# Kernel optimization log

Measured on AMD Instinct MI355X. Metric: run time of the kernel, lower is better.

Reference implementation:

```python
import jax, jax.numpy as jnp
import numpy as np

N_NODES = 100000
N_EDGES = 3200000
IN_F = 128
OUT_F = 64
HEADS = 8
ALPHA = 0.2  # LeakyReLU negative slope


def setup_inputs() -> dict:
    key = jax.random.key(0)
    k1, k2, k3, k4 = jax.random.split(key, 4)
    x = jax.random.normal(k1, (N_NODES, IN_F), dtype=jnp.float32)
    edges = jax.random.randint(k2, (2, N_EDGES), 0, N_NODES, dtype=jnp.int64)
    # glorot-uniform-ish scaled params, stacked over heads
    lim_W = np.sqrt(6.0 / (IN_F + OUT_F))
    lim_a = np.sqrt(6.0 / (2 * OUT_F + 1))
    W = jax.random.uniform(k3, (HEADS, IN_F, OUT_F), minval=-lim_W, maxval=lim_W, dtype=jnp.float32)
    a = jax.random.uniform(k4, (HEADS, 2 * OUT_F, 1), minval=-lim_a, maxval=lim_a, dtype=jnp.float32)
    return {"x": x, "edges": edges, "W": W, "a": a}


def reference(x, edges, W, a):
    # x: [N, in_f]; edges: [2, E]; W: [H, in_f, out_f]; a: [H, 2*out_f, 1]
    N = x.shape[0]
    src, tgt = edges[0], edges[1]
    outs = []
    for h in range(W.shape[0]):  # small fixed head count; keeps peak memory per-head
        Wh = x @ W[h]                                  # [N, F]
        # Whij @ a == Wh[src] @ a[:F] + Wh[tgt] @ a[F:], computed at node level
        a_src = Wh @ a[h, :OUT_F, 0]                   # [N]
        a_tgt = Wh @ a[h, OUT_F:, 0]                   # [N]
        e = -jax.nn.leaky_relu(a_src[src] + a_tgt[tgt], negative_slope=ALPHA)  # [E]
        e_exp = jnp.exp(e - jnp.max(e))                # global max, as in the torch code
        denom = jax.ops.segment_sum(e_exp, src, num_segments=N) + 1e-10  # [N]
        att = e_exp / denom[src]                       # [E] edge softmax over source groups
        msg = att[:, None] * Wh[tgt]                   # [E, F]
        outs.append(jax.ops.segment_sum(msg, src, num_segments=N))  # [N, F]
    return jnp.concatenate(outs, axis=1)               # concat reduction -> [N, H*F]
```

## Files before the change

kernel.cpp:

```cpp
#include <hip/hip_runtime.h>
#include <hip/hip_bf16.h>

#define N_NODES 100000
#define N_EDGES 3200000
#define IN_F 128
#define OUT_F 64
#define HEADS 8
#define ALPHA 0.2f

#define BSHIFT 7
#define NBUCK 782
#define CHUNK 16384
#define NPBLK 196

typedef __bf16 bf16x8 __attribute__((ext_vector_type(8)));
typedef float f32x4 __attribute__((ext_vector_type(4)));
typedef __attribute__((ext_vector_type(8))) unsigned short ushort8;

static __device__ __forceinline__ unsigned short f2b(float f) {
    __hip_bfloat16 h = __float2bfloat16(f);
    return __builtin_bit_cast(unsigned short, h);
}

static __device__ __forceinline__ void gll16(const void* g, void* l) {
    __builtin_amdgcn_global_load_lds(
        (const __attribute__((address_space(1))) void*)g,
        (__attribute__((address_space(3))) void*)l, 16, 0, 0);
}

__global__ __launch_bounds__(256) void k_prep(const float* __restrict__ W,
                                              const float* __restrict__ a,
                                              unsigned short* __restrict__ Wt,
                                              float* __restrict__ u,
                                              float* __restrict__ v,
                                              int* __restrict__ bhist) {
    int b = blockIdx.x, t = threadIdx.x;
    if (b < 256) {
        int idx = b * 256 + t;
        int k = idx & 127;
        int c = idx >> 7;
        int h = c >> 6;
        int f = c & 63;
        Wt[idx] = f2b(W[h * IN_F * OUT_F + k * OUT_F + f]);
    } else if (b == 256) {
#pragma unroll
        for (int j = 0; j < 4; ++j) {
            int t2 = t + j * 256;
            int h = t2 >> 7, k = t2 & 127;
            const float* Wrow = W + h * IN_F * OUT_F + k * OUT_F;
            const float* ah = a + h * 2 * OUT_F;
            float su = 0.f, sv = 0.f;
            for (int f = 0; f < OUT_F; ++f) {
                float wv = Wrow[f];
                su += wv * ah[f];
                sv += wv * ah[OUT_F + f];
            }
            u[t2] = su;
            v[t2] = sv;
        }
    } else {
        for (int i = t; i < NBUCK; i += 256) bhist[i] = 0;
    }
}

__global__ __launch_bounds__(256) void k_xadot(const float* __restrict__ x,
                                               const float* __restrict__ u,
                                               const float* __restrict__ v,
                                               unsigned short* __restrict__ xb,
                                               float* __restrict__ asrc,
                                               float* __restrict__ atgt) {
    int node = (blockIdx.x * 256 + threadIdx.x) >> 6;
    int lane = threadIdx.x & 63;
    if (node >= N_NODES) return;
    float2 xv = *reinterpret_cast<const float2*>(x + (size_t)node * 128 + 2 * lane);
    ushort2 pv = make_ushort2(f2b(xv.x), f2b(xv.y));
    *reinterpret_cast<ushort2*>(xb + (size_t)node * 128 + 2 * lane) = pv;
    for (int h = 0; h < 8; ++h) {
        float2 uu = *reinterpret_cast<const float2*>(u + h * 128 + 2 * lane);
        float2 vv = *reinterpret_cast<const float2*>(v + h * 128 + 2 * lane);
        float s1 = xv.x * uu.x + xv.y * uu.y;
        float s2 = xv.x * vv.x + xv.y * vv.y;
        for (int d = 1; d < 64; d <<= 1) {
            s1 += __shfl_xor(s1, d);
            s2 += __shfl_xor(s2, d);
        }
        if (lane == 0) {
            asrc[node * 8 + h] = s1;
            atgt[node * 8 + h] = s2;
        }
    }
}

__global__ __launch_bounds__(256) void k_bcount(const int* __restrict__ src,
                                                int* __restrict__ bhist) {
    __shared__ int h[NBUCK];
    for (int i = threadIdx.x; i < NBUCK; i += 256) h[i] = 0;
    __syncthreads();
    int i0 = blockIdx.x * CHUNK;
    int iend = i0 + CHUNK;
    if (iend > N_EDGES) iend = N_EDGES;
    for (int i = i0 + threadIdx.x; i < iend; i += 256)
        atomicAdd(&h[src[i] >> BSHIFT], 1);
    __syncthreads();
    for (int i = threadIdx.x; i < NBUCK; i += 256)
        if (h[i]) atomicAdd(&bhist[i], h[i]);
}

__global__ __launch_bounds__(1024) void k_bscan(const int* __restrict__ bhist,
                                                int* __restrict__ bstart,
                                                int* __restrict__ bcursor,
                                                int* __restrict__ rowptr) {
    __shared__ int s[1024];
    int t = threadIdx.x;
    int v = (t < NBUCK) ? bhist[t] : 0;
    s[t] = v;
    __syncthreads();
    for (int d = 1; d < 1024; d <<= 1) {
        int add = (t >= d) ? s[t - d] : 0;
        __syncthreads();
        s[t] += add;
        __syncthreads();
    }
    if (t < NBUCK) {
        int st = s[t] - v;
        bstart[t] = st;
        bcursor[t] = st;
    }
    if (t == 0) {
        bstart[NBUCK] = N_EDGES;
        rowptr[N_NODES] = N_EDGES;
    }
}

__global__ __launch_bounds__(256) void k_bscatter(const int* __restrict__ src,
                                                  const int* __restrict__ tgt,
                                                  int* __restrict__ bcursor,
                                                  unsigned int* __restrict__ pairs) {
    __shared__ int h[NBUCK];
    __shared__ int rsv[NBUCK];
    for (int i = threadIdx.x; i < NBUCK; i += 256) h[i] = 0;
    __syncthreads();
    int i0 = blockIdx.x * CHUNK;
    int iend = i0 + CHUNK;
    if (iend > N_EDGES) iend = N_EDGES;
    for (int i = i0 + threadIdx.x; i < iend; i += 256)
        atomicAdd(&h[src[i] >> BSHIFT], 1);
    __syncthreads();
    for (int i = threadIdx.x; i < NBUCK; i += 256) {
        int c = h[i];
        rsv[i] = c ? atomicAdd(&bcursor[i], c) : 0;
        h[i] = 0;
    }
    __syncthreads();
    for (int i = i0 + threadIdx.x; i < iend; i += 256) {
        int s = src[i];
        int b = s >> BSHIFT;
        int p = rsv[b] + atomicAdd(&h[b], 1);
        pairs[p] = ((unsigned)(s & 127) << 17) | (unsigned)tgt[i];
    }
}

__global__ __launch_bounds__(256) void k_bsort(const unsigned int* __restrict__ pairs,
                                               const int* __restrict__ bstart,
                                               int* __restrict__ rowptr,
                                               int* __restrict__ stgt) {
    __shared__ int h[128];
    __shared__ int s[128];
    int b = blockIdx.x;
    int p0 = bstart[b], p1 = bstart[b + 1];
    int n0 = b << BSHIFT;
    int t = threadIdx.x;
    if (t < 128) h[t] = 0;
    __syncthreads();
    for (int i = p0 + t; i < p1; i += 256)
        atomicAdd(&h[pairs[i] >> 17], 1);
    __syncthreads();
    int v = (t < 128) ? h[t] : 0;
    if (t < 128) s[t] = v;
    __syncthreads();
    for (int d = 1; d < 128; d <<= 1) {
        int add = (t >= d && t < 128) ? s[t - d] : 0;
        __syncthreads();
        if (t < 128) s[t] += add;
        __syncthreads();
    }
    if (t < 128) {
        int pos = p0 + s[t] - v;
        int node = n0 + t;
        if (node < N_NODES) rowptr[node] = pos;
        h[t] = pos;
    }
    __syncthreads();
    for (int i = p0 + t; i < p1; i += 256) {
        unsigned int pr = pairs[i];
        int pos = atomicAdd(&h[pr >> 17], 1);
        stgt[pos] = (int)(pr & 0x1FFFF);
    }
}

__global__ __launch_bounds__(256) void k_agg6(const int* __restrict__ rowptr,
                                              const int* __restrict__ stgt,
                                              const float* __restrict__ asrc,
                                              const float* __restrict__ atgt,
                                              const unsigned short* __restrict__ xb,
                                              unsigned short* __restrict__ aggout) {
    __shared__ char lds[4 * 2 * 5120];
    const int tid = threadIdx.x;
    const int wid = tid >> 6, lane = tid & 63;
    const int node = blockIdx.x * 4 + wid;
    if (node >= N_NODES) return;
    const int seg = lane & 15;
    const int hp = lane >> 4;
    const int base = rowptr[node], end = rowptr[node + 1];
    const float2 asr = *reinterpret_cast<const float2*>(asrc + (size_t)node * 8 + hp * 2);
    char* wbase = lds + wid * 10240;

    float2 accA[4] = {}, accB[4] = {};
    float den0 = 0.f, den1 = 0.f;

    const int deg = end - base;
    const int nch = (deg + 15) >> 4;

    auto stage = [&](char* buf, int t16) {
        int te_a = __shfl(t16, (lane & 31) >> 1);
        gll16(atgt + (size_t)te_a * 8 + (lane & 1) * 4, buf);
#pragma unroll
        for (int p = 0; p < 4; ++p) {
            int te = __shfl(t16, p * 4 + hp);
            gll16(xb + (size_t)te * 128 + seg * 8, buf + 1024 + p * 1024);
        }
    };

#define EDGE_STEP(E) { \
        uint4 xu = *reinterpret_cast<const uint4*>(Xb + (E) * 256 + seg * 16); \
        float2 w2 = *reinterpret_cast<const float2*>(buf + (E) * 32 + hp * 8); \
        float2 wA = {w2.x, w2.x}, wB = {w2.y, w2.y}; \
        _Pragma("unroll") \
        for (int i = 0; i < 4; ++i) { \
            unsigned int u = (&xu.x)[i]; \
            float2 xv; \
            xv.x = __builtin_bit_cast(float, u << 16); \
            xv.y = __builtin_bit_cast(float, u & 0xFFFF0000u); \
            asm("v_pk_fma_f32 %0, %1, %2, %0" : "+v"(accA[i]) : "v"(xv), "v"(wA)); \
            asm("v_pk_fma_f32 %0, %1, %2, %0" : "+v"(accB[i]) : "v"(xv), "v"(wB)); \
        } }

    if (nch > 0) {
        int i0 = base + seg;
        if (i0 >= end) i0 = end - 1;
        int t16 = stgt[i0];
        stage(wbase, t16);
        if (nch > 1) {
            int i1 = base + 16 + seg;
            if (i1 >= end) i1 = end - 1;
            t16 = stgt[i1];
        }
        asm volatile("s_waitcnt vmcnt(0)" ::: "memory");
        int cur = 0;
        for (int c = 0; c < nch; ++c) {
            if (c + 1 < nch) {
                stage(wbase + (cur ^ 1) * 5120, t16);
                if (c + 2 < nch) {
                    int i2 = base + (c + 2) * 16 + seg;
                    if (i2 >= end) i2 = end - 1;
                    t16 = stgt[i2];
                }
            }
            char* buf = wbase + cur * 5120;
            int c0 = base + c * 16;
            int cnt = end - c0;
            if (cnt > 16) cnt = 16;
            {
                float2 at2 = *reinterpret_cast<const float2*>(buf + seg * 32 + hp * 8);
                float z0 = asr.x + at2.x, z1 = asr.y + at2.y;
                float e0 = (z0 > 0.f) ? -z0 : -(ALPHA * z0);
                float e1 = (z1 > 0.f) ? -z1 : -(ALPHA * z1);
                bool ok = seg < cnt;
                float w0 = ok ? __expf(e0) : 0.f;
                float w1 = ok ? __expf(e1) : 0.f;
                den0 += w0;
                den1 += w1;
                float2 wout = {w0, w1};
                *reinterpret_cast<float2*>(buf + seg * 32 + hp * 8) = wout;
            }
            asm volatile("s_waitcnt lgkmcnt(0)" ::: "memory");
            __builtin_amdgcn_sched_barrier(0);
            const char* Xb = buf + 1024;
            if (cnt == 16) {
#pragma unroll 4
                for (int e = 0; e < 16; ++e) EDGE_STEP(e)
            } else {
                for (int e = 0; e < cnt; ++e) EDGE_STEP(e)
            }
            asm volatile("s_waitcnt vmcnt(0)" ::: "memory");
            cur ^= 1;
        }
    }
#undef EDGE_STEP

    for (int d = 1; d <= 8; d <<= 1) {
        den0 += __shfl_xor(den0, d);
        den1 += __shfl_xor(den1, d);
    }
    float invA = 1.f / (den0 + 1e-10f);
    float invB = 1.f / (den1 + 1e-10f);
    ushort8 oA, oB;
#pragma unroll
    for (int i = 0; i < 4; ++i) {
        oA[2 * i] = f2b(accA[i].x * invA);
        oA[2 * i + 1] = f2b(accA[i].y * invA);
        oB[2 * i] = f2b(accB[i].x * invB);
        oB[2 * i + 1] = f2b(accB[i].y * invB);
    }
    unsigned short* op = aggout + (size_t)node * 1024 + (hp * 2) * 128 + seg * 8;
    *reinterpret_cast<ushort8*>(op) = oA;
    *reinterpret_cast<ushort8*>(op + 128) = oB;
}

#define LDK2 136
__global__ __launch_bounds__(256) void k_gemm2(const unsigned short* __restrict__ agg,
                                               const unsigned short* __restrict__ Wt,
                                               float* __restrict__ out) {
    __shared__ unsigned short Al[64 * LDK2];
    __shared__ unsigned short Bl[64 * LDK2];
    const int tid = threadIdx.x;
    const int h = blockIdx.y;
    const int r0 = blockIdx.x * 64;
    for (int it = 0; it < 4; ++it) {
        int idx = tid + it * 256;
        int r = idx >> 4, k8 = (idx & 15) << 3;
        int gr = r0 + r;
        if (gr >= N_NODES) gr = N_NODES - 1;
        *reinterpret_cast<ushort8*>(&Al[r * LDK2 + k8]) =
            *reinterpret_cast<const ushort8*>(agg + (size_t)gr * 1024 + h * 128 + k8);
    }
    for (int it = 0; it < 4; ++it) {
        int idx = tid + it * 256;
        int f = idx >> 4, k8 = (idx & 15) << 3;
        *reinterpret_cast<ushort8*>(&Bl[f * LDK2 + k8]) =
            *reinterpret_cast<const ushort8*>(Wt + (size_t)(h * 64 + f) * 128 + k8);
    }
    __syncthreads();
    const int lane = tid & 63, w = tid >> 6;
    const int l15 = lane & 15, lq = lane >> 4;
    f32x4 acc[4] = {};
    for (int ks = 0; ks < 4; ++ks) {
        int koff = ks * 32 + lq * 8;
        bf16x8 af = *reinterpret_cast<const bf16x8*>(&Al[(w * 16 + l15) * LDK2 + koff]);
#pragma unroll
        for (int n = 0; n < 4; ++n) {
            bf16x8 bf_ = *reinterpret_cast<const bf16x8*>(&Bl[(n * 16 + l15) * LDK2 + koff]);
            acc[n] = __builtin_amdgcn_mfma_f32_16x16x32_bf16(af, bf_, acc[n], 0, 0, 0);
        }
    }
    for (int n = 0; n < 4; ++n) {
        int col = h * 64 + n * 16 + l15;
        int rbase = r0 + w * 16 + lq * 4;
#pragma unroll
        for (int r2 = 0; r2 < 4; ++r2) {
            int rr = rbase + r2;
            if (rr < N_NODES) out[(size_t)rr * 512 + col] = acc[n][r2];
        }
    }
}

extern "C" void kernel_launch(void* const* d_in, const int* in_sizes, int n_in,
                              void* d_out, int out_size, void* d_ws, size_t ws_size,
                              hipStream_t stream) {
    const float* x = (const float*)d_in[0];
    const int* edges = (const int*)d_in[1];
    const float* W = (const float*)d_in[2];
    const float* a = (const float*)d_in[3];
    float* out = (float*)d_out;
    const int* src = edges;
    const int* tgt = edges + N_EDGES;

    char* ws = (char*)d_ws;
    size_t off = 0;
    auto alloc = [&](size_t bytes) -> void* {
        void* p = (void*)(ws + off);
        off += (bytes + 255) & ~(size_t)255;
        return p;
    };
    unsigned short* Wt = (unsigned short*)alloc((size_t)HEADS * OUT_F * IN_F * 2);
    float* u = (float*)alloc(HEADS * IN_F * 4);
    float* v = (float*)alloc(HEADS * IN_F * 4);
    unsigned short* xb = (unsigned short*)alloc((size_t)N_NODES * IN_F * 2);
    float* asrc = (float*)alloc((size_t)N_NODES * 8 * 4);
    float* atgt = (float*)alloc((size_t)N_NODES * 8 * 4);
    int* bhist = (int*)alloc((size_t)NBUCK * 4);
    int* bstart = (int*)alloc((size_t)(NBUCK + 1) * 4);
    int* bcursor = (int*)alloc((size_t)NBUCK * 4);
    int* rowptr = (int*)alloc((size_t)(N_NODES + 1) * 4);
    unsigned int* pairs = (unsigned int*)alloc((size_t)N_EDGES * 4);
    int* stgt = (int*)alloc((size_t)N_EDGES * 4);
    (void)ws_size; (void)n_in; (void)in_sizes; (void)out_size;

    k_prep<<<258, 256, 0, stream>>>(W, a, Wt, u, v, bhist);
    k_xadot<<<25000, 256, 0, stream>>>(x, u, v, xb, asrc, atgt);
    k_bcount<<<NPBLK, 256, 0, stream>>>(src, bhist);
    k_bscan<<<1, 1024, 0, stream>>>(bhist, bstart, bcursor, rowptr);
    k_bscatter<<<NPBLK, 256, 0, stream>>>(src, tgt, bcursor, pairs);
    k_bsort<<<NBUCK, 256, 0, stream>>>(pairs, bstart, rowptr, stgt);
    k_agg6<<<25000, 256, 0, stream>>>(rowptr, stgt, asrc, atgt, xb,
                                      (unsigned short*)d_out);
    k_gemm2<<<dim3(1563, 8), 256, 0, stream>>>((const unsigned short*)d_out, Wt, out);
}
```

Baseline: 505.8 us.

## Drop double-buffered LDS staging in aggregation, use op_sel packed FMA

The aggregation kernel drops its double-buffered per-wave LDS staging and uses a single buffer, waiting on each chunk's gather before computing it. This halves LDS use per block, which may let more waves fit per CU, but removes the software overlap of the next chunk's loads with the current chunk's compute. The packed FMA now broadcasts the weight through op_sel/op_sel_hi modifiers instead of building duplicated weight registers, saving moves and registers.

Result: faster. 492.1 us (-2.7%).

```diff
diff --git a/kernel.cpp b/kernel.cpp
--- a/kernel.cpp
+++ b/kernel.cpp
@@ -198,13 +198,13 @@
     }
 }
 
-__global__ __launch_bounds__(256) void k_agg6(const int* __restrict__ rowptr,
-                                              const int* __restrict__ stgt,
-                                              const float* __restrict__ asrc,
-                                              const float* __restrict__ atgt,
-                                              const unsigned short* __restrict__ xb,
-                                              unsigned short* __restrict__ aggout) {
-    __shared__ char lds[4 * 2 * 5120];
+__global__ __launch_bounds__(256) void k_agg10(const int* __restrict__ rowptr,
+                                               const int* __restrict__ stgt,
+                                               const float* __restrict__ asrc,
+                                               const float* __restrict__ atgt,
+                                               const unsigned short* __restrict__ xb,
+                                               unsigned short* __restrict__ aggout) {
+    __shared__ char lds[4 * 5120];
     const int tid = threadIdx.x;
     const int wid = tid >> 6, lane = tid & 63;
     const int node = blockIdx.x * 4 + wid;
@@ -213,7 +213,7 @@
     const int hp = lane >> 4;
     const int base = rowptr[node], end = rowptr[node + 1];
     const float2 asr = *reinterpret_cast<const float2*>(asrc + (size_t)node * 8 + hp * 2);
-    char* wbase = lds + wid * 10240;
+    char* buf = lds + wid * 5120;
 
     float2 accA[4] = {}, accB[4] = {};
     float den0 = 0.f, den1 = 0.f;
@@ -221,7 +221,12 @@
     const int deg = end - base;
     const int nch = (deg + 15) >> 4;
 
-    auto stage = [&](char* buf, int t16) {
+    auto eidx = [&](int c) {
+        int i = base + c * 16 + seg;
+        if (i >= end) i = end - 1;
+        return i;
+    };
+    auto stage = [&](int t16) {
         int te_a = __shfl(t16, (lane & 31) >> 1);
         gll16(atgt + (size_t)te_a * 8 + (lane & 1) * 4, buf);
 #pragma unroll
@@ -234,39 +239,27 @@
 #define EDGE_STEP(E) { \
         uint4 xu = *reinterpret_cast<const uint4*>(Xb + (E) * 256 + seg * 16); \
         float2 w2 = *reinterpret_cast<const float2*>(buf + (E) * 32 + hp * 8); \
-        float2 wA = {w2.x, w2.x}, wB = {w2.y, w2.y}; \
         _Pragma("unroll") \
         for (int i = 0; i < 4; ++i) { \
             unsigned int u = (&xu.x)[i]; \
             float2 xv; \
             xv.x = __builtin_bit_cast(float, u << 16); \
             xv.y = __builtin_bit_cast(float, u & 0xFFFF0000u); \
-            asm("v_pk_fma_f32 %0, %1, %2, %0" : "+v"(accA[i]) : "v"(xv), "v"(wA)); \
-            asm("v_pk_fma_f32 %0, %1, %2, %0" : "+v"(accB[i]) : "v"(xv), "v"(wB)); \
+            asm("v_pk_fma_f32 %0, %1, %2, %0 op_sel:[0,0,0] op_sel_hi:[1,0,1]" \
+                : "+v"(accA[i]) : "v"(xv), "v"(w2)); \
+            asm("v_pk_fma_f32 %0, %1, %2, %0 op_sel:[0,1,0] op_sel_hi:[1,1,1]" \
+                : "+v"(accB[i]) : "v"(xv), "v"(w2)); \
         } }
 
     if (nch > 0) {
-        int i0 = base + seg;
-        if (i0 >= end) i0 = end - 1;
-        int t16 = stgt[i0];
-        stage(wbase, t16);
-        if (nch > 1) {
-            int i1 = base + 16 + seg;
-            if (i1 >= end) i1 = end - 1;
-            t16 = stgt[i1];
-        }
-        asm volatile("s_waitcnt vmcnt(0)" ::: "memory");
-        int cur = 0;
+        int t16 = stgt[eidx(0)];
         for (int c = 0; c < nch; ++c) {
-            if (c + 1 < nch) {
-                stage(wbase + (cur ^ 1) * 5120, t16);
-                if (c + 2 < nch) {
-                    int i2 = base + (c + 2) * 16 + seg;
-                    if (i2 >= end) i2 = end - 1;
-                    t16 = stgt[i2];
-                }
-            }
-            char* buf = wbase + cur * 5120;
+            asm volatile("s_waitcnt lgkmcnt(0)" ::: "memory");
+            __builtin_amdgcn_sched_barrier(0);
+            stage(t16);
+            if (c + 1 < nch) t16 = stgt[eidx(c + 1)];
+            asm volatile("s_waitcnt vmcnt(0)" ::: "memory");
+            __builtin_amdgcn_sched_barrier(0);
             int c0 = base + c * 16;
             int cnt = end - c0;
             if (cnt > 16) cnt = 16;
@@ -292,8 +285,6 @@
             } else {
                 for (int e = 0; e < cnt; ++e) EDGE_STEP(e)
             }
-            asm volatile("s_waitcnt vmcnt(0)" ::: "memory");
-            cur ^= 1;
         }
     }
 #undef EDGE_STEP
@@ -402,7 +393,7 @@
     k_bscan<<<1, 1024, 0, stream>>>(bhist, bstart, bcursor, rowptr);
     k_bscatter<<<NPBLK, 256, 0, stream>>>(src, tgt, bcursor, pairs);
     k_bsort<<<NBUCK, 256, 0, stream>>>(pairs, bstart, rowptr, stgt);
-    k_agg6<<<25000, 256, 0, stream>>>(rowptr, stgt, asrc, atgt, xb,
-                                      (unsigned short*)d_out);
+    k_agg10<<<25000, 256, 0, stream>>>(rowptr, stgt, asrc, atgt, xb,
+                                       (unsigned short*)d_out);
     k_gemm2<<<dim3(1563, 8), 256, 0, stream>>>((const unsigned short*)d_out, Wt, out);
 }
```
